# Kernel tuning notes

Hardware: AMD Instinct MI355X
Metric: run time of the kernel (lower is better)

The kernel has to match this reference:

```python
import jax, jax.numpy as jnp
import numpy as np

KSIZE = 3
KN = (KSIZE - 1) // 2  # 1
TEMP = 50.0


def _extract_patches(x, same_pad):
    """TF tf.image.extract_patches ordering: per location, (dy, dx, channel).
    x: [b,H,W,d] -> [b,h,w,9*d] (h=H,w=W if same_pad else H-2,W-2)."""
    if same_pad:
        x = jnp.pad(x, ((0, 0), (KN, KN), (KN, KN), (0, 0)))
    b, Hp, Wp, d = x.shape
    h, w = Hp - 2 * KN, Wp - 2 * KN
    slices = [x[:, dy:dy + h, dx:dx + w, :]
              for dy in range(KSIZE) for dx in range(KSIZE)]
    return jnp.concatenate(slices, axis=-1)


def setup_inputs() -> dict:
    key = jax.random.key(0)
    k1, k2, k3 = jax.random.split(key, 3)
    b, h, w, dims = 4, 48, 48, 64
    g_in = jax.random.normal(k1, (b, h, w, dims), dtype=jnp.float32)
    # binary inpainting mask (1 = known background, 0 = hole)
    mask = (jax.random.uniform(k2, (b, h, w, 1)) > 0.5).astype(jnp.float32)
    W2 = jax.random.normal(k3, (2 * dims, dims), dtype=jnp.float32) / np.sqrt(2.0 * dims)
    b2 = jnp.zeros((dims,), dtype=jnp.float32)
    return {"g_in": g_in, "mask": mask, "W2": W2, "b2": b2}


def reference(g_in, mask, W2, b2):
    b, h, w, dims = g_in.shape
    c = (h - 2 * KN) * (w - 2 * KN)

    mask_r = mask  # already (h,w,1); broadcasts over dims (== tile)
    bg = g_in * mask_r

    # p1: VALID 3x3 patches of bg -> dynamic kernels, [b, c, 9*dims]
    p1 = _extract_patches(bg, same_pad=False).reshape(b, c, KSIZE * KSIZE * dims)
    # p2: SAME 3x3 patches of g_in, [b, h, w, 9*dims]
    p2 = _extract_patches(g_in, same_pad=True)

    # cross-correlation: conv2d(ft, k1) == per-location dot with each bg patch
    CS = jnp.einsum('byxk,bjk->byxj', p2, p1)              # [b,h,w,c]
    k1d = jnp.sum(p1 * p1, axis=2)                          # [b,c]
    wwd = jnp.sum(p2 * p2, axis=3, keepdims=True)           # [b,h,w,1]
    DS1 = k1d[:, None, None, :] + wwd - 2.0 * CS            # squared distances
    mu = jnp.mean(DS1, axis=3, keepdims=True)
    sd = jnp.std(DS1, axis=3, keepdims=True)                # population std (tf.math.reduce_std)
    DS2 = -jnp.tanh((DS1 - mu) / sd)
    CA = jax.nn.softmax(TEMP * DS2, axis=-1)                # [b,h,w,c]

    # transposed conv aggregation with per-sample kernels k2[b,j,dy,dx,ch]
    k2 = p1.reshape(b, c, KSIZE, KSIZE, dims)
    CA_pad = jnp.pad(CA, ((0, 0), (KN, KN), (KN, KN), (0, 0)))
    acl = jnp.zeros((b, h, w, dims), dtype=g_in.dtype)
    for dy in range(KSIZE):
        for dx in range(KSIZE):
            win = CA_pad[:, 2 * KN - dy:2 * KN - dy + h, 2 * KN - dx:2 * KN - dx + w, :]
            acl = acl + jnp.einsum('byxj,bjd->byxd', win, k2[:, :, dy, dx, :])
    acl = acl / 9.0

    ACL = bg + acl * (1.0 - mask_r)
    con1 = jnp.concatenate([g_in, ACL], axis=3)             # [b,h,w,2*dims]
    return jax.nn.elu(jnp.einsum('byxk,kd->byxd', con1, W2) + b2)
```

## Files before the change

kernel.cpp:

```cpp
#include <hip/hip_runtime.h>
#include <hip/hip_fp16.h>
#include <math.h>

#define BB 4
#define HH 48
#define WW 48
#define DD 64
#define CH 46
#define CWp 46
#define CC (CH*CWp)
#define KK 576
#define HWp (HH*WW)
#define PW 50
#define PP (PW*PW)

#define SLOTW 48
#define NSLOT 2208
#define NGRP 276
#define KPAD NSLOT
#define KSPLIT0 1120
#define QW 2304
#define QROWS 2500

typedef __attribute__((ext_vector_type(8))) short short8;
typedef __attribute__((ext_vector_type(4))) float float4v;

#define OFFB_GPAD  ((size_t)0)
#define OFFB_BGPAD ((size_t)1280000)
#define OFFB_E     ((size_t)2560000)
#define OFFB_K1D   ((size_t)2596864)
#define OFFB_P1T   ((size_t)2632192)
#define OFFB_S     ((size_t)12806656)
#define OFFB_AGG0  ((size_t)53504512)
#define OFFB_AGG1  ((size_t)64121344)
#define OFFB_Q     ((size_t)74738176)

__device__ __forceinline__ ushort f2bf(float x) {
    unsigned u = __float_as_uint(x);
    return (ushort)((u + 0x7FFFu + ((u >> 16) & 1u)) >> 16);
}

__device__ __forceinline__ float waveReduceSum(float x) {
#pragma unroll
    for (int o = 32; o > 0; o >>= 1) x += __shfl_down(x, o, 64);
    return x;
}

__device__ __forceinline__ __half2 u2h2(uint u) {
    union { uint u; __half2 h; } c; c.u = u; return c.h;
}

__device__ __forceinline__ uint cvtpk_bf16(float lo, float hi) {
    uint r;
    asm("v_cvt_pk_bf16_f32 %0, %1, %2" : "=v"(r) : "v"(lo), "v"(hi));
    return r;
}

__device__ __forceinline__ float softexp(float d, float mu, float isd) {
    float z = (d - mu) * isd;
    float E2 = __expf(z + z);
    float r = __builtin_amdgcn_rcpf(E2 + 1.f);
    return __expf(fmaf(100.f, r, -50.f));
}

typedef __attribute__((address_space(3))) void lds_void_t;
typedef __attribute__((address_space(1))) void gmem_void_t;
__device__ __forceinline__ void gld16(const ushort* g, ushort* lds) {
    __builtin_amdgcn_global_load_lds((gmem_void_t*)g, (lds_void_t*)lds, 16, 0, 0);
}

__global__ __launch_bounds__(256) void build_pads(const float* __restrict__ g,
                                                  const float* __restrict__ mask,
                                                  ushort* __restrict__ gpad,
                                                  ushort* __restrict__ bgpad,
                                                  float* __restrict__ e) {
    int w = threadIdx.x >> 6, c = threadIdx.x & 63;
    int q4 = blockIdx.x * 4 + w;
    int b = q4 / PP, q = q4 % PP;
    int yp = q / PW, xp = q % PW;
    size_t o = (size_t)q4 * DD + c;
    if (yp >= 1 && yp <= HH && xp >= 1 && xp <= WW) {
        int pix = (yp - 1) * WW + (xp - 1);
        float gv = g[((size_t)b * HWp + pix) * DD + c];
        float m  = mask[(size_t)b * HWp + pix];
        float bgv = gv * m;
        gpad[o]  = f2bf(gv);
        bgpad[o] = f2bf(bgv);
        float ss = waveReduceSum(bgv * bgv);
        if (c == 0) e[b * HWp + pix] = ss;
    } else {
        gpad[o] = 0;
        bgpad[o] = 0;
    }
}

__global__ __launch_bounds__(256) void build_p1t(const ushort* __restrict__ bgpad,
                                                 const float* __restrict__ e,
                                                 ushort* __restrict__ p1t,
                                                 float* __restrict__ k1d) {
    int d9 = blockIdx.y, b = blockIdx.z;
    int t = threadIdx.x;
    if (blockIdx.x == 35) {
        int jg = (b * 9 + d9) * 256 + t;
        if (jg < BB * NSLOT) {
            int bb = jg / NSLOT, st = jg - bb * NSLOT;
            int jy = st / SLOTW, jx = st - jy * SLOTW;
            float s = 0.f;
            if (jx < CWp) {
                const float* eb = e + bb * HWp + jy * WW + jx;
#pragma unroll
                for (int ddy = 0; ddy < 3; ddy++)
#pragma unroll
                    for (int ddx = 0; ddx < 3; ddx++) s += eb[ddy * WW + ddx];
            }
            k1d[jg] = s;
        }
        return;
    }
    __shared__ ushort T[64 * 65];
    int jt = blockIdx.x;
    int dy = d9 / 3, dx = d9 - dy * 3;
    const ushort* src = bgpad + (size_t)b * PP * DD;
    int lr = t >> 3, c8 = (t & 7) * 8;
#pragma unroll
    for (int pass = 0; pass < 2; pass++) {
        int r = lr + pass * 32;
        int st = jt * 64 + r;
        int jy = st / SLOTW, jx = st - jy * SLOTW;
        uint4 d = make_uint4(0, 0, 0, 0);
        if (jx < CWp && jy < CWp)
            d = *(const uint4*)(src + (size_t)((jy + dy + 1) * PW + (jx + dx + 1)) * DD + c8);
        ushort tmp[8];
        *(uint4*)tmp = d;
#pragma unroll
        for (int u = 0; u < 8; u++) T[r * 65 + c8 + u] = tmp[u];
    }
    __syncthreads();
#pragma unroll
    for (int pass = 0; pass < 2; pass++) {
        int c = lr + pass * 32;
        int j8 = (t & 7) * 8;
        int col0 = jt * 64 + j8;
        ushort tmp[8];
#pragma unroll
        for (int u = 0; u < 8; u++) tmp[u] = T[(j8 + u) * 65 + c];
        if (col0 < NSLOT)
            *(uint4*)(p1t + ((size_t)b * KK + d9 * 64 + c) * NSLOT + col0) = *(const uint4*)tmp;
    }
}

__global__ __launch_bounds__(256) void qgemm(const ushort* __restrict__ gpad,
                                             const ushort* __restrict__ bgpad,
                                             __half* __restrict__ Qout) {
    __shared__ ushort As[2 * 4096];
    __shared__ ushort Bs[2 * 4096];
    int i0 = blockIdx.x;
    int b = (i0 & 7) >> 1;
    int tile = ((i0 >> 3) << 1) | (i0 & 1);
    int ty = tile / 18, tx = tile - ty * 18;
    int m0 = ty * 128, n0 = tx * 128;
    const ushort* Ag = gpad + (size_t)b * PP * DD;
    const ushort* Bg = bgpad + (size_t)b * PP * DD;

    int tid = threadIdx.x;
    int l = tid & 63, w = tid >> 6;
    int quad = l >> 4, l15 = l & 15;
    int sw8 = (l15 >> 1) & 3;
    int wm = (w >> 1) * 64, wn = (w & 1) * 64;
    int rowInC = l >> 2;
    int cSw = (l & 3) ^ ((l >> 3) & 3);

#pragma unroll
    for (int i = 0; i < 2; i++) {
        int rg = w * 2 + i;
        int r = rg * 16 + rowInC;
        int u = m0 + r; if (u > QROWS - 1) u = QROWS - 1;
        int n = n0 + r;
        int vy = n / 48, vx = n - vy * 48;
        int baseA = u * DD + cSw * 8;
        int baseB = ((vy + 1) * PW + (vx + 1)) * DD + cSw * 8;
        gld16(Ag + baseA, As + rg * 512);
        gld16(Bg + baseB, Bs + rg * 512);
        gld16(Ag + baseA + 32, As + 4096 + rg * 512);
        gld16(Bg + baseB + 32, Bs + 4096 + rg * 512);
    }
    float4v acc[4][4];
#pragma unroll
    for (int i = 0; i < 4; i++)
#pragma unroll
        for (int j = 0; j < 4; j++) acc[i][j] = (float4v){0.f, 0.f, 0.f, 0.f};
    __syncthreads();
#pragma unroll
    for (int kb = 0; kb < 2; kb++) {
        const ushort* Ax = As + kb * 4096;
        const ushort* Bx = Bs + kb * 4096;
        short8 af[4], bf[4];
#pragma unroll
        for (int i = 0; i < 4; i++)
            af[i] = *(const short8*)&Ax[(wm + i * 16 + l15) * 32 + ((quad ^ sw8)) * 8];
#pragma unroll
        for (int j = 0; j < 4; j++)
            bf[j] = *(const short8*)&Bx[(wn + j * 16 + l15) * 32 + ((quad ^ sw8)) * 8];
#pragma unroll
        for (int i = 0; i < 4; i++)
#pragma unroll
            for (int j = 0; j < 4; j++)
                acc[i][j] = __builtin_amdgcn_mfma_f32_16x16x32_bf16(af[i], bf[j], acc[i][j], 0, 0, 0);
    }
    __half* C = Qout + (size_t)b * QROWS * QW;
#pragma unroll
    for (int i = 0; i < 4; i++) {
#pragma unroll
        for (int j = 0; j < 4; j++) {
            int n = n0 + wn + j * 16 + l15;
#pragma unroll
            for (int r = 0; r < 4; r++) {
                int m = m0 + wm + i * 16 + quad * 4 + r;
                if (m < QROWS) C[(size_t)m * QW + n] = __float2half(acc[i][j][r]);
            }
        }
    }
}

__global__ __launch_bounds__(320) void qrowsoft2(const __half* __restrict__ Q,
                                                 const float* __restrict__ k1d,
                                                 ushort* __restrict__ CA) {
    __shared__ float red[16][321];
    int i0 = blockIdx.x;
    int z = i0 & 7;
    int b = z >> 1;
    int sub = ((i0 >> 3) << 1) | (i0 & 1);
    int y = sub / 6, xt = sub - y * 6;
    int x0 = xt * 8;

    int t = threadIdx.x;
    bool act = (t < NGRP);
    int jy = t / 6, jxb = (t - jy * 6) * 8;
    int slot0 = jy * SLOTW + jxb;
    bool vc6 = act && (jxb == 40);

    __half2 acc[8][4];
#pragma unroll
    for (int p = 0; p < 8; p++)
#pragma unroll
        for (int k = 0; k < 4; k++) acc[p][k] = u2h2(0u);

    float k1v[8] = {0.f, 0.f, 0.f, 0.f, 0.f, 0.f, 0.f, 0.f};

    if (act) {
        const float* k1 = k1d + (size_t)b * NSLOT + slot0;
        float4 ka = *(const float4*)k1;
        float4 kb = *(const float4*)(k1 + 4);
        k1v[0] = ka.x; k1v[1] = ka.y; k1v[2] = ka.z; k1v[3] = ka.w;
        k1v[4] = kb.x; k1v[5] = kb.y; k1v[6] = kb.z; k1v[7] = kb.w;

#pragma unroll 1
        for (int dy = 0; dy < 3; dy++) {
            const __half* rp = Q + ((size_t)b * QROWS + (size_t)(y + dy) * PW + x0) * QW
                               + slot0 + dy * 48;
            uint4 W4[10]; uint W1[10];
#pragma unroll
            for (int d = 0; d < 10; d++) {
                const __half* pr = rp + (size_t)d * QW;
                W4[d] = *(const uint4*)pr;
                W1[d] = *(const uint*)(pr + 8);
            }
#pragma unroll
            for (int d = 0; d < 10; d++) {
                uint w0 = W4[d].x, w1 = W4[d].y, w2 = W4[d].z, w3 = W4[d].w, w4 = W1[d];
                if (d < 8) {
                    acc[d][0] = __hadd2(acc[d][0], u2h2(w0));
                    acc[d][1] = __hadd2(acc[d][1], u2h2(w1));
                    acc[d][2] = __hadd2(acc[d][2], u2h2(w2));
                    acc[d][3] = __hadd2(acc[d][3], u2h2(w3));
                }
                if (d >= 1 && d <= 8) {
                    uint s0 = (w0 >> 16) | (w1 << 16);
                    uint s1 = (w1 >> 16) | (w2 << 16);
                    uint s2 = (w2 >> 16) | (w3 << 16);
                    uint s3 = (w3 >> 16) | (w4 << 16);
                    acc[d-1][0] = __hadd2(acc[d-1][0], u2h2(s0));
                    acc[d-1][1] = __hadd2(acc[d-1][1], u2h2(s1));
                    acc[d-1][2] = __hadd2(acc[d-1][2], u2h2(s2));
                    acc[d-1][3] = __hadd2(acc[d-1][3], u2h2(s3));
                }
                if (d >= 2) {
                    acc[d-2][0] = __hadd2(acc[d-2][0], u2h2(w1));
                    acc[d-2][1] = __hadd2(acc[d-2][1], u2h2(w2));
                    acc[d-2][2] = __hadd2(acc[d-2][2], u2h2(w3));
                    acc[d-2][3] = __hadd2(acc[d-2][3], u2h2(w4));
                }
            }
        }
    }

    if (vc6) {
#pragma unroll
        for (int p = 0; p < 8; p++) acc[p][3] = u2h2(0u);
    }

#pragma unroll
    for (int p = 0; p < 8; p++) {
        float s1p = 0.f, s2p = 0.f;
#pragma unroll
        for (int k = 0; k < 4; k++) {
            float2 f = __half22float2(acc[p][k]);
            float d0 = k1v[2*k]   - 2.f * f.x;
            float d1 = k1v[2*k+1] - 2.f * f.y;
            s1p += d0 + d1;
            s2p = fmaf(d0, d0, fmaf(d1, d1, s2p));
        }
        red[p][t] = s1p;
        red[8 + p][t] = s2p;
    }
    __syncthreads();
    if (t < 256) {
        int v = t >> 4, sb = t & 15;
        float s = 0.f;
#pragma unroll
        for (int k = 0; k < 20; k++) s += red[v][sb + 16 * k];
#pragma unroll
        for (int o = 8; o > 0; o >>= 1) s += __shfl_down(s, o, 16);
        if (sb == 0) red[v][320] = s;
    }
    __syncthreads();
    float mu[8], isd[8];
#pragma unroll
    for (int p = 0; p < 8; p++) {
        float m = red[p][320] * (1.f / (float)CC);
        float ex2 = red[8 + p][320] * (1.f / (float)CC);
        mu[p] = m;
        isd[p] = rsqrtf(ex2 - m * m);
    }

    uint eb[8][4];
#pragma unroll
    for (int p = 0; p < 8; p++) {
        float es = 0.f;
#pragma unroll
        for (int k = 0; k < 4; k++) {
            float2 f = __half22float2(acc[p][k]);
            float d0 = k1v[2*k]   - 2.f * f.x;
            float d1 = k1v[2*k+1] - 2.f * f.y;
            if (k == 3 && vc6) { d0 = 1e9f; d1 = 1e9f; }
            float e0 = softexp(d0, mu[p], isd[p]);
            float e1 = softexp(d1, mu[p], isd[p]);
            es += e0 + e1;
            eb[p][k] = cvtpk_bf16(e0, e1);
        }
        red[p][t] = act ? es : 0.f;
    }
    __syncthreads();
    if (t < 128) {
        int v = t >> 4, sb = t & 15;
        float s = 0.f;
#pragma unroll
        for (int k = 0; k < 20; k++) s += red[v][sb + 16 * k];
#pragma unroll
        for (int o = 8; o > 0; o >>= 1) s += __shfl_down(s, o, 16);
        if (sb == 0) red[v][320] = s;
    }
    __syncthreads();

    if (act) {
#pragma unroll
        for (int p = 0; p < 8; p++) {
            float iz = __builtin_amdgcn_rcpf(red[p][320]);
            uint o[4];
#pragma unroll
            for (int k = 0; k < 4; k++) {
                uint w = eb[p][k];
                float lo = __uint_as_float(w << 16) * iz;
                float hi = __uint_as_float(w & 0xffff0000u) * iz;
                o[k] = cvtpk_bf16(lo, hi);
            }
            int pix = y * WW + x0 + p;
            ushort* wp = CA + ((size_t)b * HWp + pix) * (size_t)NSLOT + slot0;
            *(uint4*)wp = *(const uint4*)o;
        }
    }
}

template <int NF, bool NMASK>
__device__ __forceinline__ void gemm_tile_db(const ushort* __restrict__ Ab,
                                             const ushort* __restrict__ Bb,
                                             int lda, int ldb, int kb, int ke,
                                             int Nrem,
                                             ushort* As, ushort* Bs,
                                             float4v (&acc)[4][NF]) {
    constexpr int NBI = NF / 2;
    constexpr int BBUF = 2048 * NBI;
    int tid = threadIdx.x;
    int l = tid & 63, w = tid >> 6;
    int quad = l >> 4, l15 = l & 15;
    int sw8 = (l15 >> 1) & 3;
    int wm = (w >> 1) * 64, wn = (w & 1) * (NF * 16);
    int rowInC = l >> 2;
    int cSw = (l & 3) ^ ((l >> 3) & 3);

#pragma unroll
    for (int i = 0; i < 2; i++) {
        int rg = w * 2 + i;
        gld16(Ab + (size_t)(rg * 16 + rowInC) * lda + kb + cSw * 8, As + rg * 512);
    }
#pragma unroll
    for (int i = 0; i < NBI; i++) {
        int rg = w * NBI + i;
        int r = rg * 16 + rowInC;
        if (!NMASK || r < Nrem)
            gld16(Bb + (size_t)r * ldb + kb + cSw * 8, Bs + rg * 512);
    }

    int buf = 0;
    for (int k0 = kb; k0 < ke; k0 += 32) {
        __syncthreads();
        int nb = buf ^ 1;
        if (k0 + 32 < ke) {
#pragma unroll
            for (int i = 0; i < 2; i++) {
                int rg = w * 2 + i;
                gld16(Ab + (size_t)(rg * 16 + rowInC) * lda + (k0 + 32) + cSw * 8,
                      As + nb * 4096 + rg * 512);
            }
#pragma unroll
            for (int i = 0; i < NBI; i++) {
                int rg = w * NBI + i;
                int r = rg * 16 + rowInC;
                if (!NMASK || r < Nrem)
                    gld16(Bb + (size_t)r * ldb + (k0 + 32) + cSw * 8,
                          Bs + nb * BBUF + rg * 512);
            }
        }
        const ushort* Ax = As + buf * 4096;
        const ushort* Bx = Bs + buf * BBUF;
        short8 af[4], bf[NF];
#pragma unroll
        for (int i = 0; i < 4; i++)
            af[i] = *(const short8*)&Ax[(wm + i * 16 + l15) * 32 + ((quad ^ sw8)) * 8];
#pragma unroll
        for (int j = 0; j < NF; j++)
            bf[j] = *(const short8*)&Bx[(wn + j * 16 + l15) * 32 + ((quad ^ sw8)) * 8];
#pragma unroll
        for (int i = 0; i < 4; i++)
#pragma unroll
            for (int j = 0; j < NF; j++)
                acc[i][j] = __builtin_amdgcn_mfma_f32_16x16x32_bf16(af[i], bf[j], acc[i][j], 0, 0, 0);
        buf = nb;
    }
}

__global__ __launch_bounds__(256) void gemm2_split(const ushort* __restrict__ A,
                                                   const ushort* __restrict__ Bt,
                                                   __half* __restrict__ agg0,
                                                   __half* __restrict__ agg1) {
    __shared__ ushort As[2 * 4096];
    __shared__ ushort Bs[2 * 6144];
    int i0 = blockIdx.x;
    int z = i0 & 7;
    int b = z >> 1, split = z & 1;
    int tile = i0 >> 3;
    int ty = tile / 3, tx = tile - ty * 3;
    int m0 = ty * 128, n0 = tx * 192;
    const ushort* Ab = A + (size_t)b * HWp * KPAD + (size_t)m0 * KPAD;
    const ushort* Bb = Bt + (size_t)b * KK * KPAD + (size_t)n0 * KPAD;
    float4v acc[4][6];
#pragma unroll
    for (int i = 0; i < 4; i++)
#pragma unroll
        for (int j = 0; j < 6; j++) acc[i][j] = (float4v){0.f, 0.f, 0.f, 0.f};

    gemm_tile_db<6, false>(Ab, Bb, KPAD, KPAD, split ? KSPLIT0 : 0,
                           split ? KPAD : KSPLIT0, 192, As, Bs, acc);

    int tid = threadIdx.x;
    int lane = tid & 63, wid = tid >> 6;
    int quad = lane >> 4, l15 = lane & 15;
    int wm = (wid >> 1) * 64, wn = (wid & 1) * 96;
    __half* C = (split ? agg1 : agg0) + (size_t)b * HWp * KK;
#pragma unroll
    for (int i = 0; i < 4; i++) {
#pragma unroll
        for (int j = 0; j < 6; j++) {
            int n = n0 + wn + j * 16 + l15;
#pragma unroll
            for (int r = 0; r < 4; r++) {
                int m = m0 + wm + i * 16 + quad * 4 + r;
                C[(size_t)m * KK + n] = __float2half(acc[i][j][r]);
            }
        }
    }
}

__global__ __launch_bounds__(256) void final_k(const float* __restrict__ g,
                                               const float* __restrict__ mask,
                                               const __half* __restrict__ agg0,
                                               const __half* __restrict__ agg1,
                                               const float* __restrict__ W2,
                                               const float* __restrict__ b2,
                                               float* __restrict__ out) {
    int w = threadIdx.x >> 6, d = threadIdx.x & 63;
    int pix = blockIdx.x * 4 + w;
    int b = pix / HWp, yx = pix % HWp;
    int y = yx / WW, x = yx % WW;

    __shared__ float con1[4][128];
    float acl = 0.f;
#pragma unroll
    for (int dy = 0; dy < 3; dy++) {
#pragma unroll
        for (int dx = 0; dx < 3; dx++) {
            int yy = y + 1 - dy, xx = x + 1 - dx;
            if (yy >= 0 && yy < HH && xx >= 0 && xx < WW) {
                size_t off = ((size_t)(b * HWp + yy * WW + xx)) * KK + (dy * 3 + dx) * DD + d;
                acl += __half2float(agg0[off]) + __half2float(agg1[off]);
            }
        }
    }
    float m = mask[pix];
    float gv = g[(size_t)pix * DD + d];
    float bgv = gv * m;
    float ACL = bgv + (acl / 9.f) * (1.f - m);
    con1[w][d] = gv;
    con1[w][64 + d] = ACL;
    __syncthreads();
    float accv = b2[d];
#pragma unroll 8
    for (int k = 0; k < 128; k++) accv = fmaf(con1[w][k], W2[k * 64 + d], accv);
    out[(size_t)pix * DD + d] = accv > 0.f ? accv : expm1f(accv);
}

extern "C" void kernel_launch(void* const* d_in, const int* in_sizes, int n_in,
                              void* d_out, int out_size, void* d_ws, size_t ws_size,
                              hipStream_t stream) {
    const float* g    = (const float*)d_in[0];
    const float* mask = (const float*)d_in[1];
    const float* W2   = (const float*)d_in[2];
    const float* b2   = (const float*)d_in[3];
    float* out = (float*)d_out;
    char* ws = (char*)d_ws;

    ushort* gpad  = (ushort*)(ws + OFFB_GPAD);
    ushort* bgpad = (ushort*)(ws + OFFB_BGPAD);
    float*  e     = (float*) (ws + OFFB_E);
    float*  k1d   = (float*) (ws + OFFB_K1D);
    ushort* p1t   = (ushort*)(ws + OFFB_P1T);
    ushort* CA    = (ushort*)(ws + OFFB_S);
    __half* agg0  = (__half*)(ws + OFFB_AGG0);
    __half* agg1  = (__half*)(ws + OFFB_AGG1);
    __half* Qbuf  = (__half*)(ws + OFFB_Q);

    build_pads<<<BB * PP / 4, 256, 0, stream>>>(g, mask, gpad, bgpad, e);
    build_p1t<<<dim3(36, 9, BB), 256, 0, stream>>>(bgpad, e, p1t, k1d);

    qgemm<<<1440, 256, 0, stream>>>(gpad, bgpad, Qbuf);
    qrowsoft2<<<BB * HWp / 8, 320, 0, stream>>>(Qbuf, k1d, CA);

    gemm2_split<<<432, 256, 0, stream>>>(CA, p1t, agg0, agg1);

    final_k<<<BB * HWp / 4, 256, 0, stream>>>(g, mask, agg0, agg1, W2, b2, out);
}
```

Measured before the change: 182.2 us.

## Replace 9x-wide aggregation GEMM with 2D box-summed attention times background GEMM

The transposed-conv aggregation is re-expressed algebraically. Each output pixel's acl equals a sum over bg pixels weighted by a 3x3 box-summed attention map. A new boxsumW kernel builds that box-summed CA in fp16, and gemm3 multiplies it against a transposed bg matrix with K=64 output columns. The old version ran a 576-wide GEMM and then did a 9-tap gather in the final kernel. The change shrinks GEMM FLOPs about 9x and removes the large agg buffers. The cost is an extra box-sum pass over the full CA matrix, an 8-way split-K with fp32 partial sums, and a switch from bf16 to fp16 for CA and bg, which changes precision. qrowsoft also processes 4 pixels per block instead of 8.

```diff
diff --git a/kernel.cpp b/kernel.cpp
--- a/kernel.cpp
+++ b/kernel.cpp
@@ -17,23 +17,22 @@
 #define SLOTW 48
 #define NSLOT 2208
 #define NGRP 276
-#define KPAD NSLOT
-#define KSPLIT0 1120
 #define QW 2304
 #define QROWS 2500
 
 typedef __attribute__((ext_vector_type(8))) short short8;
+typedef __attribute__((ext_vector_type(8))) _Float16 half8;
 typedef __attribute__((ext_vector_type(4))) float float4v;
 
 #define OFFB_GPAD  ((size_t)0)
 #define OFFB_BGPAD ((size_t)1280000)
 #define OFFB_E     ((size_t)2560000)
 #define OFFB_K1D   ((size_t)2596864)
-#define OFFB_P1T   ((size_t)2632192)
-#define OFFB_S     ((size_t)12806656)
-#define OFFB_AGG0  ((size_t)53504512)
-#define OFFB_AGG1  ((size_t)64121344)
-#define OFFB_Q     ((size_t)74738176)
+#define OFFB_BGT   ((size_t)2632192)
+#define OFFB_Q     ((size_t)3811840)
+#define OFFB_S     ((size_t)49891840)
+#define OFFB_W     ((size_t)90589696)
+#define OFFB_ACL   ((size_t)133057024)
 
 __device__ __forceinline__ ushort f2bf(float x) {
     unsigned u = __float_as_uint(x);
@@ -94,58 +93,56 @@
     }
 }
 
-__global__ __launch_bounds__(256) void build_p1t(const ushort* __restrict__ bgpad,
-                                                 const float* __restrict__ e,
-                                                 ushort* __restrict__ p1t,
-                                                 float* __restrict__ k1d) {
-    int d9 = blockIdx.y, b = blockIdx.z;
+__global__ __launch_bounds__(256) void build_bgt_k1d(const ushort* __restrict__ bgpad,
+                                                     const float* __restrict__ e,
+                                                     ushort* __restrict__ bgT,
+                                                     float* __restrict__ k1d) {
+    int b = blockIdx.y;
     int t = threadIdx.x;
-    if (blockIdx.x == 35) {
-        int jg = (b * 9 + d9) * 256 + t;
-        if (jg < BB * NSLOT) {
-            int bb = jg / NSLOT, st = jg - bb * NSLOT;
+    if (blockIdx.x == 36) {
+#pragma unroll 1
+        for (int st = t; st < NSLOT; st += 256) {
             int jy = st / SLOTW, jx = st - jy * SLOTW;
             float s = 0.f;
             if (jx < CWp) {
-                const float* eb = e + bb * HWp + jy * WW + jx;
+                const float* eb = e + (size_t)b * HWp + jy * WW + jx;
 #pragma unroll
                 for (int ddy = 0; ddy < 3; ddy++)
 #pragma unroll
                     for (int ddx = 0; ddx < 3; ddx++) s += eb[ddy * WW + ddx];
             }
-            k1d[jg] = s;
+            k1d[(size_t)b * NSLOT + st] = s;
         }
         return;
     }
     __shared__ ushort T[64 * 65];
     int jt = blockIdx.x;
-    int dy = d9 / 3, dx = d9 - dy * 3;
     const ushort* src = bgpad + (size_t)b * PP * DD;
     int lr = t >> 3, c8 = (t & 7) * 8;
 #pragma unroll
     for (int pass = 0; pass < 2; pass++) {
         int r = lr + pass * 32;
-        int st = jt * 64 + r;
-        int jy = st / SLOTW, jx = st - jy * SLOTW;
-        uint4 d = make_uint4(0, 0, 0, 0);
-        if (jx < CWp && jy < CWp)
-            d = *(const uint4*)(src + (size_t)((jy + dy + 1) * PW + (jx + dx + 1)) * DD + c8);
+        int v = jt * 64 + r;
+        int vy = v / 48, vx = v - vy * 48;
+        uint4 d = *(const uint4*)(src + (size_t)((vy + 1) * PW + (vx + 1)) * DD + c8);
         ushort tmp[8];
         *(uint4*)tmp = d;
 #pragma unroll
-        for (int u = 0; u < 8; u++) T[r * 65 + c8 + u] = tmp[u];
+        for (int u = 0; u < 8; u++) {
+            float f = __uint_as_float((uint)tmp[u] << 16);
+            __half h = __float2half_rn(f);
+            T[r * 65 + c8 + u] = *(ushort*)&h;
+        }
     }
     __syncthreads();
 #pragma unroll
     for (int pass = 0; pass < 2; pass++) {
         int c = lr + pass * 32;
         int j8 = (t & 7) * 8;
-        int col0 = jt * 64 + j8;
         ushort tmp[8];
 #pragma unroll
         for (int u = 0; u < 8; u++) tmp[u] = T[(j8 + u) * 65 + c];
-        if (col0 < NSLOT)
-            *(uint4*)(p1t + ((size_t)b * KK + d9 * 64 + c) * NSLOT + col0) = *(const uint4*)tmp;
+        *(uint4*)(bgT + ((size_t)b * 64 + c) * QW + jt * 64 + j8) = *(const uint4*)tmp;
     }
 }
 
@@ -222,16 +219,15 @@
     }
 }
 
-__global__ __launch_bounds__(320) void qrowsoft2(const __half* __restrict__ Q,
+__global__ __launch_bounds__(320) void qrowsoft3(const __half* __restrict__ Q,
                                                  const float* __restrict__ k1d,
                                                  ushort* __restrict__ CA) {
-    __shared__ float red[16][321];
+    __shared__ float red[8][321];
     int i0 = blockIdx.x;
-    int z = i0 & 7;
-    int b = z >> 1;
+    int b = (i0 & 7) >> 1;
     int sub = ((i0 >> 3) << 1) | (i0 & 1);
-    int y = sub / 6, xt = sub - y * 6;
-    int x0 = xt * 8;
+    int y = sub / 12, xt = sub - y * 12;
+    int x0 = xt * 4;
 
     int t = threadIdx.x;
     bool act = (t < NGRP);
@@ -239,9 +235,9 @@
     int slot0 = jy * SLOTW + jxb;
     bool vc6 = act && (jxb == 40);
 
-    __half2 acc[8][4];
-#pragma unroll
-    for (int p = 0; p < 8; p++)
+    __half2 acc[4][4];
+#pragma unroll
+    for (int p = 0; p < 4; p++)
 #pragma unroll
         for (int k = 0; k < 4; k++) acc[p][k] = u2h2(0u);
 
@@ -258,23 +254,23 @@
         for (int dy = 0; dy < 3; dy++) {
             const __half* rp = Q + ((size_t)b * QROWS + (size_t)(y + dy) * PW + x0) * QW
                                + slot0 + dy * 48;
-            uint4 W4[10]; uint W1[10];
-#pragma unroll
-            for (int d = 0; d < 10; d++) {
+            uint4 W4[6]; uint W1[6];
+#pragma unroll
+            for (int d = 0; d < 6; d++) {
                 const __half* pr = rp + (size_t)d * QW;
                 W4[d] = *(const uint4*)pr;
                 W1[d] = *(const uint*)(pr + 8);
             }
 #pragma unroll
-            for (int d = 0; d < 10; d++) {
+            for (int d = 0; d < 6; d++) {
                 uint w0 = W4[d].x, w1 = W4[d].y, w2 = W4[d].z, w3 = W4[d].w, w4 = W1[d];
-                if (d < 8) {
+                if (d < 4) {
                     acc[d][0] = __hadd2(acc[d][0], u2h2(w0));
                     acc[d][1] = __hadd2(acc[d][1], u2h2(w1));
                     acc[d][2] = __hadd2(acc[d][2], u2h2(w2));
                     acc[d][3] = __hadd2(acc[d][3], u2h2(w3));
                 }
-                if (d >= 1 && d <= 8) {
+                if (d >= 1 && d <= 4) {
                     uint s0 = (w0 >> 16) | (w1 << 16);
                     uint s1 = (w1 >> 16) | (w2 << 16);
                     uint s2 = (w2 >> 16) | (w3 << 16);
@@ -296,11 +292,11 @@
 
     if (vc6) {
 #pragma unroll
-        for (int p = 0; p < 8; p++) acc[p][3] = u2h2(0u);
-    }
-
-#pragma unroll
-    for (int p = 0; p < 8; p++) {
+        for (int p = 0; p < 4; p++) acc[p][3] = u2h2(0u);
+    }
+
+#pragma unroll
+    for (int p = 0; p < 4; p++) {
         float s1p = 0.f, s2p = 0.f;
 #pragma unroll
         for (int k = 0; k < 4; k++) {
@@ -311,10 +307,10 @@
             s2p = fmaf(d0, d0, fmaf(d1, d1, s2p));
         }
         red[p][t] = s1p;
-        red[8 + p][t] = s2p;
-    }
-    __syncthreads();
-    if (t < 256) {
+        red[4 + p][t] = s2p;
+    }
+    __syncthreads();
+    if (t < 128) {
         int v = t >> 4, sb = t & 15;
         float s = 0.f;
 #pragma unroll
@@ -324,18 +320,18 @@
         if (sb == 0) red[v][320] = s;
     }
     __syncthreads();
-    float mu[8], isd[8];
-#pragma unroll
-    for (int p = 0; p < 8; p++) {
+    float mu[4], isd[4];
+#pragma unroll
+    for (int p = 0; p < 4; p++) {
         float m = red[p][320] * (1.f / (float)CC);
-        float ex2 = red[8 + p][320] * (1.f / (float)CC);
+        float ex2 = red[4 + p][320] * (1.f / (float)CC);
         mu[p] = m;
         isd[p] = rsqrtf(ex2 - m * m);
     }
 
-    uint eb[8][4];
-#pragma unroll
-    for (int p = 0; p < 8; p++) {
+    uint eb[4][4];
+#pragma unroll
+    for (int p = 0; p < 4; p++) {
         float es = 0.f;
 #pragma unroll
         for (int k = 0; k < 4; k++) {
@@ -351,7 +347,7 @@
         red[p][t] = act ? es : 0.f;
     }
     __syncthreads();
-    if (t < 128) {
+    if (t < 64) {
         int v = t >> 4, sb = t & 15;
         float s = 0.f;
 #pragma unroll
@@ -364,15 +360,16 @@
 
     if (act) {
 #pragma unroll
-        for (int p = 0; p < 8; p++) {
+        for (int p = 0; p < 4; p++) {
             float iz = __builtin_amdgcn_rcpf(red[p][320]);
             uint o[4];
 #pragma unroll
             for (int k = 0; k < 4; k++) {
-                uint w = eb[p][k];
-                float lo = __uint_as_float(w << 16) * iz;
-                float hi = __uint_as_float(w & 0xffff0000u) * iz;
-                o[k] = cvtpk_bf16(lo, hi);
+                uint wv = eb[p][k];
+                float lo = __uint_as_float(wv << 16) * iz;
+                float hi = __uint_as_float(wv & 0xffff0000u) * iz;
+                __half2 hh = __halves2half2(__float2half_rn(lo), __float2half_rn(hi));
+                o[k] = *(uint*)&hh;
             }
             int pix = y * WW + x0 + p;
             ushort* wp = CA + ((size_t)b * HWp + pix) * (size_t)NSLOT + slot0;
@@ -381,35 +378,118 @@
     }
 }
 
-template <int NF, bool NMASK>
-__device__ __forceinline__ void gemm_tile_db(const ushort* __restrict__ Ab,
-                                             const ushort* __restrict__ Bb,
-                                             int lda, int ldb, int kb, int ke,
-                                             int Nrem,
-                                             ushort* As, ushort* Bs,
-                                             float4v (&acc)[4][NF]) {
-    constexpr int NBI = NF / 2;
-    constexpr int BBUF = 2048 * NBI;
+__global__ __launch_bounds__(320) void boxsumW(const ushort* __restrict__ CAu,
+                                               ushort* __restrict__ Wout) {
+    int i0 = blockIdx.x;
+    int b = (i0 & 7) >> 1;
+    int sub = ((i0 >> 3) << 1) | (i0 & 1);
+    int y = sub / 12, xt = sub - y * 12;
+    int x0 = xt * 4;
+
+    int t = threadIdx.x;
+    if (t >= 288) return;
+    int vy = t / 6, vx0 = (t - vy * 6) * 8;
+
+    __half2 acc[4][4];
+#pragma unroll
+    for (int p = 0; p < 4; p++)
+#pragma unroll
+        for (int k = 0; k < 4; k++) acc[p][k] = u2h2(0u);
+
+#pragma unroll
+    for (int dy = 0; dy < 3; dy++) {
+        int yy = y + 1 - dy;
+        int jyv = vy - dy;
+        if (yy < 0 || yy >= 48 || jyv < 0 || jyv >= 46) continue;
+        const ushort* rp = CAu + (size_t)b * HWp * (size_t)NSLOT
+                         + (ptrdiff_t)((yy * 48 + x0 - 1) * NSLOT + jyv * 48 + vx0 - 2);
+        uint4 W4[6]; uint W1[6];
+#pragma unroll
+        for (int d = 0; d < 6; d++) {
+            int xp = x0 - 1 + d;
+            if (xp >= 0 && xp < 48) {
+                W4[d] = *(const uint4*)(rp + (size_t)d * NSLOT);
+                W1[d] = *(const uint*)(rp + (size_t)d * NSLOT + 8);
+            } else {
+                W4[d] = make_uint4(0u, 0u, 0u, 0u); W1[d] = 0u;
+            }
+        }
+#pragma unroll
+        for (int d = 0; d < 6; d++) {
+            uint w0 = W4[d].x, w1 = W4[d].y, w2 = W4[d].z, w3 = W4[d].w, w4 = W1[d];
+            if (vx0 == 0) w0 = 0u;
+            if (d < 4) {
+                acc[d][0] = __hadd2(acc[d][0], u2h2(w0));
+                acc[d][1] = __hadd2(acc[d][1], u2h2(w1));
+                acc[d][2] = __hadd2(acc[d][2], u2h2(w2));
+                acc[d][3] = __hadd2(acc[d][3], u2h2(w3));
+            }
+            if (d >= 1 && d <= 4) {
+                uint s0 = (w0 >> 16) | (w1 << 16);
+                uint s1 = (w1 >> 16) | (w2 << 16);
+                uint s2 = (w2 >> 16) | (w3 << 16);
+                uint s3 = (w3 >> 16) | (w4 << 16);
+                acc[d-1][0] = __hadd2(acc[d-1][0], u2h2(s0));
+                acc[d-1][1] = __hadd2(acc[d-1][1], u2h2(s1));
+                acc[d-1][2] = __hadd2(acc[d-1][2], u2h2(s2));
+                acc[d-1][3] = __hadd2(acc[d-1][3], u2h2(s3));
+            }
+            if (d >= 2) {
+                acc[d-2][0] = __hadd2(acc[d-2][0], u2h2(w1));
+                acc[d-2][1] = __hadd2(acc[d-2][1], u2h2(w2));
+                acc[d-2][2] = __hadd2(acc[d-2][2], u2h2(w3));
+                acc[d-2][3] = __hadd2(acc[d-2][3], u2h2(w4));
+            }
+        }
+    }
+
+#pragma unroll
+    for (int p = 0; p < 4; p++) {
+        uint o[4];
+#pragma unroll
+        for (int k = 0; k < 4; k++) {
+            __half2 h = acc[p][k];
+            o[k] = *(uint*)&h;
+        }
+        size_t row = (size_t)b * HWp + (size_t)(y * 48 + x0 + p);
+        *(uint4*)(Wout + row * QW + vy * 48 + vx0) = *(const uint4*)o;
+    }
+}
+
+__global__ __launch_bounds__(256) void gemm3(const ushort* __restrict__ Wm,
+                                             const ushort* __restrict__ bgT,
+                                             float* __restrict__ aclp) {
+    __shared__ ushort As[2 * 4096];
+    __shared__ ushort Bs[2 * 2048];
+    int i0 = blockIdx.x;
+    int s = i0 & 7;
+    int b = (i0 >> 3) & 3;
+    int mt = i0 >> 5;
+    int m0 = mt * 128;
+    int kb = s * 288, ke = kb + 288;
+    const ushort* Ab = Wm + ((size_t)b * HWp + m0) * QW;
+    const ushort* Bb = bgT + (size_t)b * 64 * QW;
+
     int tid = threadIdx.x;
     int l = tid & 63, w = tid >> 6;
     int quad = l >> 4, l15 = l & 15;
     int sw8 = (l15 >> 1) & 3;
-    int wm = (w >> 1) * 64, wn = (w & 1) * (NF * 16);
+    int wm = w * 32;
     int rowInC = l >> 2;
     int cSw = (l & 3) ^ ((l >> 3) & 3);
 
+    float4v acc[2][4];
+#pragma unroll
+    for (int i = 0; i < 2; i++)
+#pragma unroll
+        for (int j = 0; j < 4; j++) acc[i][j] = (float4v){0.f, 0.f, 0.f, 0.f};
+
 #pragma unroll
     for (int i = 0; i < 2; i++) {
         int rg = w * 2 + i;
-        gld16(Ab + (size_t)(rg * 16 + rowInC) * lda + kb + cSw * 8, As + rg * 512);
-    }
-#pragma unroll
-    for (int i = 0; i < NBI; i++) {
-        int rg = w * NBI + i;
-        int r = rg * 16 + rowInC;
-        if (!NMASK || r < Nrem)
-            gld16(Bb + (size_t)r * ldb + kb + cSw * 8, Bs + rg * 512);
-    }
+        gld16(Ab + (size_t)(rg * 16 + rowInC) * QW + kb + cSw * 8, As + rg * 512);
+    }
+    gld16(Bb + (size_t)(w * 16 + rowInC) * QW + kb + cSw * 8, Bs + w * 512);
 
     int buf = 0;
     for (int k0 = kb; k0 < ke; k0 += 32) {
@@ -419,103 +499,57 @@
 #pragma unroll
             for (int i = 0; i < 2; i++) {
                 int rg = w * 2 + i;
-                gld16(Ab + (size_t)(rg * 16 + rowInC) * lda + (k0 + 32) + cSw * 8,
+                gld16(Ab + (size_t)(rg * 16 + rowInC) * QW + (k0 + 32) + cSw * 8,
                       As + nb * 4096 + rg * 512);
             }
-#pragma unroll
-            for (int i = 0; i < NBI; i++) {
-                int rg = w * NBI + i;
-                int r = rg * 16 + rowInC;
-                if (!NMASK || r < Nrem)
-                    gld16(Bb + (size_t)r * ldb + (k0 + 32) + cSw * 8,
-                          Bs + nb * BBUF + rg * 512);
-            }
+            gld16(Bb + (size_t)(w * 16 + rowInC) * QW + (k0 + 32) + cSw * 8,
+                  Bs + nb * 2048 + w * 512);
         }
         const ushort* Ax = As + buf * 4096;
-        const ushort* Bx = Bs + buf * BBUF;
-        short8 af[4], bf[NF];
-#pragma unroll
-        for (int i = 0; i < 4; i++)
-            af[i] = *(const short8*)&Ax[(wm + i * 16 + l15) * 32 + ((quad ^ sw8)) * 8];
-#pragma unroll
-        for (int j = 0; j < NF; j++)
-            bf[j] = *(const short8*)&Bx[(wn + j * 16 + l15) * 32 + ((quad ^ sw8)) * 8];
-#pragma unroll
-        for (int i = 0; i < 4; i++)
-#pragma unroll
-            for (int j = 0; j < NF; j++)
-                acc[i][j] = __builtin_amdgcn_mfma_f32_16x16x32_bf16(af[i], bf[j], acc[i][j], 0, 0, 0);
+        const ushort* Bx = Bs + buf * 2048;
+        half8 af[2], bf[4];
+#pragma unroll
+        for (int i = 0; i < 2; i++)
+            af[i] = *(const half8*)&Ax[(wm + i * 16 + l15) * 32 + ((quad ^ sw8)) * 8];
+#pragma unroll
+        for (int j = 0; j < 4; j++)
+            bf[j] = *(const half8*)&Bx[(j * 16 + l15) * 32 + ((quad ^ sw8)) * 8];
+#pragma unroll
+        for (int i = 0; i < 2; i++)
+#pragma unroll
+            for (int j = 0; j < 4; j++)
+                acc[i][j] = __builtin_amdgcn_mfma_f32_16x16x32_f16(af[i], bf[j], acc[i][j], 0, 0, 0);
         buf = nb;
     }
-}
-
-__global__ __launch_bounds__(256) void gemm2_split(const ushort* __restrict__ A,
-                                                   const ushort* __restrict__ Bt,
-                                                   __half* __restrict__ agg0,
-                                                   __half* __restrict__ agg1) {
-    __shared__ ushort As[2 * 4096];
-    __shared__ ushort Bs[2 * 6144];
-    int i0 = blockIdx.x;
-    int z = i0 & 7;
-    int b = z >> 1, split = z & 1;
-    int tile = i0 >> 3;
-    int ty = tile / 3, tx = tile - ty * 3;
-    int m0 = ty * 128, n0 = tx * 192;
-    const ushort* Ab = A + (size_t)b * HWp * KPAD + (size_t)m0 * KPAD;
-    const ushort* Bb = Bt + (size_t)b * KK * KPAD + (size_t)n0 * KPAD;
-    float4v acc[4][6];
-#pragma unroll
-    for (int i = 0; i < 4; i++)
-#pragma unroll
-        for (int j = 0; j < 6; j++) acc[i][j] = (float4v){0.f, 0.f, 0.f, 0.f};
-
-    gemm_tile_db<6, false>(Ab, Bb, KPAD, KPAD, split ? KSPLIT0 : 0,
-                           split ? KPAD : KSPLIT0, 192, As, Bs, acc);
-
-    int tid = threadIdx.x;
-    int lane = tid & 63, wid = tid >> 6;
-    int quad = lane >> 4, l15 = lane & 15;
-    int wm = (wid >> 1) * 64, wn = (wid & 1) * 96;
-    __half* C = (split ? agg1 : agg0) + (size_t)b * HWp * KK;
-#pragma unroll
-    for (int i = 0; i < 4; i++) {
-#pragma unroll
-        for (int j = 0; j < 6; j++) {
-            int n = n0 + wn + j * 16 + l15;
+
+    float* C = aclp + ((size_t)s * (BB * HWp) + (size_t)b * HWp) * 64;
+#pragma unroll
+    for (int i = 0; i < 2; i++)
+#pragma unroll
+        for (int j = 0; j < 4; j++)
 #pragma unroll
             for (int r = 0; r < 4; r++) {
                 int m = m0 + wm + i * 16 + quad * 4 + r;
-                C[(size_t)m * KK + n] = __float2half(acc[i][j][r]);
-            }
-        }
-    }
-}
-
-__global__ __launch_bounds__(256) void final_k(const float* __restrict__ g,
-                                               const float* __restrict__ mask,
-                                               const __half* __restrict__ agg0,
-                                               const __half* __restrict__ agg1,
-                                               const float* __restrict__ W2,
-                                               const float* __restrict__ b2,
-                                               float* __restrict__ out) {
+                int n = j * 16 + l15;
+                C[(size_t)m * 64 + n] = acc[i][j][r];
+            }
+}
+
+__global__ __launch_bounds__(256) void final_k2(const float* __restrict__ g,
+                                                const float* __restrict__ mask,
+                                                const float* __restrict__ aclp,
+                                                const float* __restrict__ W2,
+                                                const float* __restrict__ b2,
+                                                float* __restrict__ out) {
     int w = threadIdx.x >> 6, d = threadIdx.x & 63;
     int pix = blockIdx.x * 4 + w;
-    int b = pix / HWp, yx = pix % HWp;
-    int y = yx / WW, x = yx % WW;
 
     __shared__ float con1[4][128];
     float acl = 0.f;
-#pragma unroll
-    for (int dy = 0; dy < 3; dy++) {
-#pragma unroll
-        for (int dx = 0; dx < 3; dx++) {
-            int yy = y + 1 - dy, xx = x + 1 - dx;
-            if (yy >= 0 && yy < HH && xx >= 0 && xx < WW) {
-                size_t off = ((size_t)(b * HWp + yy * WW + xx)) * KK + (dy * 3 + dx) * DD + d;
-                acl += __half2float(agg0[off]) + __half2float(agg1[off]);
-            }
-        }
-    }
+    const float* ap = aclp + (size_t)pix * 64 + d;
+#pragma unroll
+    for (int s = 0; s < 8; s++) acl += ap[(size_t)s * (BB * HWp) * 64];
+
     float m = mask[pix];
     float gv = g[(size_t)pix * DD + d];
     float bgv = gv * m;
@@ -543,19 +577,20 @@
     ushort* bgpad = (ushort*)(ws + OFFB_BGPAD);
     float*  e     = (float*) (ws + OFFB_E);
     float*  k1d   = (float*) (ws + OFFB_K1D);
-    ushort* p1t   = (ushort*)(ws + OFFB_P1T);
+    ushort* bgT   = (ushort*)(ws + OFFB_BGT);
+    __half* Qbuf  = (__half*)(ws + OFFB_Q);
     ushort* CA    = (ushort*)(ws + OFFB_S);
-    __half* agg0  = (__half*)(ws + OFFB_AGG0);
-    __half* agg1  = (__half*)(ws + OFFB_AGG1);
-    __half* Qbuf  = (__half*)(ws + OFFB_Q);
+    ushort* Wbuf  = (ushort*)(ws + OFFB_W);
+    float*  aclp  = (float*) (ws + OFFB_ACL);
 
     build_pads<<<BB * PP / 4, 256, 0, stream>>>(g, mask, gpad, bgpad, e);
-    build_p1t<<<dim3(36, 9, BB), 256, 0, stream>>>(bgpad, e, p1t, k1d);
+    build_bgt_k1d<<<dim3(37, BB), 256, 0, stream>>>(bgpad, e, bgT, k1d);
 
     qgemm<<<1440, 256, 0, stream>>>(gpad, bgpad, Qbuf);
-    qrowsoft2<<<BB * HWp / 8, 320, 0, stream>>>(Qbuf, k1d, CA);
-
-    gemm2_split<<<432, 256, 0, stream>>>(CA, p1t, agg0, agg1);
-
-    final_k<<<BB * HWp / 4, 256, 0, stream>>>(g, mask, agg0, agg1, W2, b2, out);
-}
+    qrowsoft3<<<BB * HWp / 4, 320, 0, stream>>>(Qbuf, k1d, CA);
+
+    boxsumW<<<BB * HWp / 4, 320, 0, stream>>>(CA, Wbuf);
+    gemm3<<<576, 256, 0, stream>>>(Wbuf, bgT, aclp);
+
+    final_k2<<<BB * HWp / 4, 256, 0, stream>>>(g, mask, aclp, W2, b2, out);
+}
```

Result: faster. 167.7 us (-7.9%).
